# Optimization experiments

Measured on AMD Instinct MI355X. Metric: run time of the kernel, lower is better.

Reference implementation:

```python
import jax, jax.numpy as jnp
import numpy as np

N = 100000        # nodes
E = 1600000       # directed edges (avg degree 16)
F_IN, F_HID, F_OUT = 512, 32, 16


def setup_inputs() -> dict:
    key = jax.random.key(0)
    k0, k1, k2, k3 = jax.random.split(key, 4)
    x = jax.random.normal(k0, (N, F_IN), dtype=jnp.float32)
    edge_index = jax.random.randint(k1, (2, E), 0, N, dtype=jnp.int32)
    # Glorot-ish init for the two GCNConv linear weights
    W1 = jax.random.normal(k2, (F_IN, F_HID), dtype=jnp.float32) / np.float32(np.sqrt(F_IN))
    W2 = jax.random.normal(k3, (F_HID, F_OUT), dtype=jnp.float32) / np.float32(np.sqrt(F_HID))
    b1 = jnp.zeros((F_HID,), jnp.float32)
    b2 = jnp.zeros((F_OUT,), jnp.float32)
    return {"x": x, "W1": W1, "b1": b1, "W2": W2, "b2": b2, "edge_index": edge_index}


def gcn_conv(x, W, b, src, dst):
    """PyG GCNConv: h = x W; symmetric-normalized aggregation with self-loops; + bias."""
    h = x @ W                                   # [N, F_out] project first (PyG order)
    # degree including the implicit self-loop (start from ones)
    deg = jnp.ones((N,), h.dtype).at[dst].add(1.0)
    dinv = jax.lax.rsqrt(deg)                   # deg^{-1/2}
    coef = (dinv[src] * dinv[dst])[:, None]     # [E, 1] edge norm
    msg = h[src] * coef                         # gather + scale
    agg = jax.ops.segment_sum(msg, dst, num_segments=N)  # scatter-add to dst
    agg = agg + h * (dinv * dinv)[:, None]      # self-loop contribution
    return agg + b


def reference(x, W1, b1, W2, b2, edge_index):
    src, dst = edge_index[0], edge_index[1]
    h = jax.nn.relu(gcn_conv(x, W1, b1, src, dst))
    # F.dropout(training=self.training) is identity in eval mode
    h = gcn_conv(h, W2, b2, src, dst)
    return jax.nn.log_softmax(h, axis=1)
```

## Files before the change

### kernel.cpp

```cpp
#include <hip/hip_runtime.h>
#include <hip/hip_bf16.h>
#include <cstdint>

#define NN   100000
#define NE   1600000
#define FIN  512
#define FHID 32
#define FOUT 16

#define BSHIFT 8
#define BSIZE  256
#define NBUCK  391
#define EPB    2048
#define NCHUNK ((NE + EPB - 1) / EPB)

typedef float f32x4 __attribute__((ext_vector_type(4)));
typedef short s16x8 __attribute__((ext_vector_type(8)));
typedef short s16x4 __attribute__((ext_vector_type(4)));
typedef int   i32x4 __attribute__((ext_vector_type(4)));
typedef unsigned int u32;
typedef unsigned short u16;

__device__ __forceinline__ short f2bf(float f) {
  union { float f; uint32_t u; } v; v.f = f;
  uint32_t r = v.u + 0x7fffu + ((v.u >> 16) & 1u);
  return (short)(r >> 16);
}
__device__ __forceinline__ float bf2f(u16 u) {
  union { uint32_t u; float f; } v; v.u = (uint32_t)u << 16; return v.f;
}

__global__ __launch_bounds__(256) void k_hist(const int* __restrict__ dst,
                                              u32* __restrict__ bcount) {
  __shared__ u32 h[NBUCK];
  int tid = threadIdx.x;
  for (int i = tid; i < NBUCK; i += 256) h[i] = 0;
  __syncthreads();
  int base = blockIdx.x * EPB;
  #pragma unroll
  for (int i = 0; i < 2; ++i) {
    int e0 = base + (i * 256 + tid) * 4;
    if (e0 + 3 < NE) {
      i32x4 d4 = *(const i32x4*)(dst + e0);
      atomicAdd(&h[d4[0] >> BSHIFT], 1u);
      atomicAdd(&h[d4[1] >> BSHIFT], 1u);
      atomicAdd(&h[d4[2] >> BSHIFT], 1u);
      atomicAdd(&h[d4[3] >> BSHIFT], 1u);
    } else {
      for (int k = 0; k < 4; ++k)
        if (e0 + k < NE) atomicAdd(&h[dst[e0 + k] >> BSHIFT], 1u);
    }
  }
  __syncthreads();
  for (int i = tid; i < NBUCK; i += 256)
    if (h[i]) atomicAdd(&bcount[i], h[i]);
}

__global__ __launch_bounds__(512) void k_bscan(const u32* __restrict__ bc,
                                               u32* __restrict__ bstart,
                                               u32* __restrict__ bcur) {
  __shared__ u32 tmp[512];
  int tid = threadIdx.x;
  u32 v = (tid < NBUCK) ? bc[tid] : 0;
  tmp[tid] = v;
  __syncthreads();
  #pragma unroll
  for (int off = 1; off < 512; off <<= 1) {
    u32 t = (tid >= off) ? tmp[tid - off] : 0;
    __syncthreads();
    tmp[tid] += t;
    __syncthreads();
  }
  if (tid < NBUCK) { u32 e = tmp[tid] - v; bstart[tid] = e; bcur[tid] = e; }
  if (tid == 511) bstart[NBUCK] = tmp[511];
}

__global__ __launch_bounds__(512) void k_bin(const int* __restrict__ src,
                                             const int* __restrict__ dst,
                                             u32* __restrict__ bcur,
                                             u32* __restrict__ binned) {
  __shared__ u32 cnt[NBUCK];
  __shared__ u32 lofs[NBUCK];
  __shared__ u32 gbase[NBUCK];
  __shared__ u32 tmp[512];
  __shared__ u32 stage[EPB];
  __shared__ u16 sb[EPB];
  int tid = threadIdx.x;
  for (int i = tid; i < NBUCK; i += 512) cnt[i] = 0;
  __syncthreads();

  int base = blockIdx.x * EPB;
  int e0 = base + tid * 4;
  u32 vals[4];
  u32 ofs[4];
  int bks[4];
  if (e0 + 3 < NE) {
    i32x4 s4 = *(const i32x4*)(src + e0);
    i32x4 d4 = *(const i32x4*)(dst + e0);
    #pragma unroll
    for (int k = 0; k < 4; ++k) {
      int b = d4[k] >> BSHIFT;
      bks[k] = b;
      vals[k] = (u32)s4[k] | ((u32)(d4[k] & (BSIZE - 1)) << 17);
      ofs[k] = atomicAdd(&cnt[b], 1u);
    }
  } else {
    #pragma unroll
    for (int k = 0; k < 4; ++k) {
      int e = e0 + k;
      bool ok = e < NE;
      int s = 0, d = 0;
      if (ok) { s = src[e]; d = dst[e]; }
      int b = ok ? (d >> BSHIFT) : -1;
      bks[k] = b;
      vals[k] = (u32)s | ((u32)(d & (BSIZE - 1)) << 17);
      ofs[k] = ok ? atomicAdd(&cnt[b], 1u) : 0;
    }
  }
  __syncthreads();

  u32 cv = (tid < NBUCK) ? cnt[tid] : 0;
  tmp[tid] = cv;
  __syncthreads();
  #pragma unroll
  for (int off = 1; off < 512; off <<= 1) {
    u32 t = (tid >= off) ? tmp[tid - off] : 0;
    __syncthreads();
    tmp[tid] += t;
    __syncthreads();
  }
  if (tid < NBUCK) {
    lofs[tid] = tmp[tid] - cv;
    gbase[tid] = cv ? atomicAdd(&bcur[tid], cv) : 0;
  }
  __syncthreads();
  u32 total = tmp[511];
  __syncthreads();

  #pragma unroll
  for (int k = 0; k < 4; ++k) {
    if (bks[k] >= 0) {
      u32 sl = lofs[bks[k]] + ofs[k];
      stage[sl] = vals[k];
      sb[sl] = (u16)bks[k];
    }
  }
  __syncthreads();

  for (u32 s2 = tid; s2 < total; s2 += 512) {
    int b = sb[s2];
    binned[gbase[b] + (s2 - lofs[b])] = stage[s2];
  }
}

__global__ __launch_bounds__(256) void k_fin(const u32* __restrict__ binned,
                                             const u32* __restrict__ bstart,
                                             int* __restrict__ deg,
                                             int* __restrict__ rs,
                                             float* __restrict__ dinv,
                                             int* __restrict__ csr) {
  __shared__ u32 degl[BSIZE];
  __shared__ u32 rsl[BSIZE];
  int tid = threadIdx.x;
  int b = blockIdx.x;
  u32 start = bstart[b];
  u32 n = bstart[b + 1] - start;

  degl[tid] = 0;
  __syncthreads();
  for (u32 k = tid; k < n; k += 256)
    atomicAdd(&degl[binned[start + k] >> 17], 1u);
  __syncthreads();

  u32 v = degl[tid];
  rsl[tid] = v;
  __syncthreads();
  #pragma unroll
  for (int off = 1; off < 256; off <<= 1) {
    u32 t = (tid >= off) ? rsl[tid - off] : 0;
    __syncthreads();
    rsl[tid] += t;
    __syncthreads();
  }
  u32 e = rsl[tid] - v;
  __syncthreads();
  rsl[tid] = e;

  int g = b * BSIZE + tid;
  if (g < NN) {
    deg[g] = (int)v;
    rs[g] = (int)(start + e);
    dinv[g] = rsqrtf(1.0f + (float)v);
  }
  __syncthreads();

  for (u32 k = tid; k < n; k += 256) {
    u32 vv = binned[start + k];
    u32 pos = atomicAdd(&rsl[vv >> 17], 1u);
    csr[start + pos] = (int)(vv & 0x1FFFFu);
  }
}

__global__ __launch_bounds__(256) void k_gemm1(const float* __restrict__ x,
                                               const float* __restrict__ W1,
                                               const float* __restrict__ dinv,
                                               u16* __restrict__ Hs1) {
  __shared__ s16x8 Blds[16][2][64];
  const int tid = threadIdx.x;
  for (int it = 0; it < 64; ++it) {
    int flat = it * 256 + tid;
    int i  = flat & 7;
    int l  = (flat >> 3) & 63;
    int nt = (flat >> 9) & 1;
    int kt = flat >> 10;
    int k  = kt * 32 + ((l >> 4) << 3) + i;
    int n  = nt * 16 + (l & 15);
    ((short*)Blds)[flat] = f2bf(W1[k * 32 + n]);
  }
  __syncthreads();

  const int lane = tid & 63;
  const int wv   = tid >> 6;
  const int h    = lane >> 4;
  const int m    = lane & 15;
  const int wid  = blockIdx.x * 4 + wv;
  if (wid >= 3125) return;
  const int t0 = wid * 2;

  const float* xr0 = x + (size_t)(t0 * 16 + m) * FIN + h * 8;
  const float* xr1 = xr0 + (size_t)16 * FIN;

  f32x4 acc[2][2] = {};
  #pragma unroll
  for (int kt = 0; kt < 16; ++kt) {
    f32x4 a0 = *(const f32x4*)(xr0 + kt * 32);
    f32x4 a1 = *(const f32x4*)(xr0 + kt * 32 + 4);
    f32x4 c0 = *(const f32x4*)(xr1 + kt * 32);
    f32x4 c1 = *(const f32x4*)(xr1 + kt * 32 + 4);
    s16x8 b0 = Blds[kt][0][lane];
    s16x8 b1 = Blds[kt][1][lane];
    s16x8 af, cf;
    af[0]=f2bf(a0[0]); af[1]=f2bf(a0[1]); af[2]=f2bf(a0[2]); af[3]=f2bf(a0[3]);
    af[4]=f2bf(a1[0]); af[5]=f2bf(a1[1]); af[6]=f2bf(a1[2]); af[7]=f2bf(a1[3]);
    cf[0]=f2bf(c0[0]); cf[1]=f2bf(c0[1]); cf[2]=f2bf(c0[2]); cf[3]=f2bf(c0[3]);
    cf[4]=f2bf(c1[0]); cf[5]=f2bf(c1[1]); cf[6]=f2bf(c1[2]); cf[7]=f2bf(c1[3]);
    acc[0][0] = __builtin_amdgcn_mfma_f32_16x16x32_bf16(af, b0, acc[0][0], 0, 0, 0);
    acc[0][1] = __builtin_amdgcn_mfma_f32_16x16x32_bf16(af, b1, acc[0][1], 0, 0, 0);
    acc[1][0] = __builtin_amdgcn_mfma_f32_16x16x32_bf16(cf, b0, acc[1][0], 0, 0, 0);
    acc[1][1] = __builtin_amdgcn_mfma_f32_16x16x32_bf16(cf, b1, acc[1][1], 0, 0, 0);
  }
  #pragma unroll
  for (int rt = 0; rt < 2; ++rt) {
    #pragma unroll
    for (int r = 0; r < 4; ++r) {
      int row = (t0 + rt) * 16 + h * 4 + r;
      float di = dinv[row];
      u16* o = Hs1 + (size_t)row * FHID + m;
      o[0]  = (u16)f2bf(acc[rt][0][r] * di);
      o[16] = (u16)f2bf(acc[rt][1][r] * di);
    }
  }
}

__global__ __launch_bounds__(256) void k_gat1(const int* __restrict__ csr,
                                              const int* __restrict__ rs,
                                              const int* __restrict__ deg,
                                              const float* __restrict__ dinv,
                                              const float* __restrict__ b1,
                                              const float* __restrict__ W2,
                                              const u16* __restrict__ Hs1,
                                              u16* __restrict__ Hs2) {
  __shared__ float w[FHID * FOUT];
  for (int i = threadIdx.x; i < FHID * FOUT; i += 256) w[i] = W2[i];
  __syncthreads();

  int t = blockIdx.x * 256 + threadIdx.x;
  int d = t >> 2;
  if (d >= NN) return;
  int p = t & 3;
  int start = rs[d], n = deg[d];

  float a0[8], a1[8], a2[8], a3[8];
  {
    s16x8 v = *(const s16x8*)(Hs1 + (size_t)d * FHID + p * 8);
    #pragma unroll
    for (int k = 0; k < 8; ++k) {
      a0[k] = bf2f((u16)v[k]); a1[k] = 0.f; a2[k] = 0.f; a3[k] = 0.f;
    }
  }
  int j = 0;
  for (; j + 8 <= n; j += 8) {
    int s0 = csr[start + j];
    int s1 = csr[start + j + 1];
    int s2 = csr[start + j + 2];
    int s3 = csr[start + j + 3];
    int s4 = csr[start + j + 4];
    int s5 = csr[start + j + 5];
    int s6 = csr[start + j + 6];
    int s7 = csr[start + j + 7];
    s16x8 v0 = *(const s16x8*)(Hs1 + (size_t)s0 * FHID + p * 8);
    s16x8 v1 = *(const s16x8*)(Hs1 + (size_t)s1 * FHID + p * 8);
    s16x8 v2 = *(const s16x8*)(Hs1 + (size_t)s2 * FHID + p * 8);
    s16x8 v3 = *(const s16x8*)(Hs1 + (size_t)s3 * FHID + p * 8);
    s16x8 v4 = *(const s16x8*)(Hs1 + (size_t)s4 * FHID + p * 8);
    s16x8 v5 = *(const s16x8*)(Hs1 + (size_t)s5 * FHID + p * 8);
    s16x8 v6 = *(const s16x8*)(Hs1 + (size_t)s6 * FHID + p * 8);
    s16x8 v7 = *(const s16x8*)(Hs1 + (size_t)s7 * FHID + p * 8);
    #pragma unroll
    for (int k = 0; k < 8; ++k) {
      a0[k] += bf2f((u16)v0[k]);
      a1[k] += bf2f((u16)v1[k]);
      a2[k] += bf2f((u16)v2[k]);
      a3[k] += bf2f((u16)v3[k]);
      a0[k] += bf2f((u16)v4[k]);
      a1[k] += bf2f((u16)v5[k]);
      a2[k] += bf2f((u16)v6[k]);
      a3[k] += bf2f((u16)v7[k]);
    }
  }
  for (; j + 4 <= n; j += 4) {
    int s0 = csr[start + j];
    int s1 = csr[start + j + 1];
    int s2 = csr[start + j + 2];
    int s3 = csr[start + j + 3];
    s16x8 v0 = *(const s16x8*)(Hs1 + (size_t)s0 * FHID + p * 8);
    s16x8 v1 = *(const s16x8*)(Hs1 + (size_t)s1 * FHID + p * 8);
    s16x8 v2 = *(const s16x8*)(Hs1 + (size_t)s2 * FHID + p * 8);
    s16x8 v3 = *(const s16x8*)(Hs1 + (size_t)s3 * FHID + p * 8);
    #pragma unroll
    for (int k = 0; k < 8; ++k) {
      a0[k] += bf2f((u16)v0[k]);
      a1[k] += bf2f((u16)v1[k]);
      a2[k] += bf2f((u16)v2[k]);
      a3[k] += bf2f((u16)v3[k]);
    }
  }
  for (; j < n; ++j) {
    int s0 = csr[start + j];
    s16x8 v0 = *(const s16x8*)(Hs1 + (size_t)s0 * FHID + p * 8);
    #pragma unroll
    for (int k = 0; k < 8; ++k) a0[k] += bf2f((u16)v0[k]);
  }

  float dd = dinv[d];
  float h[8];
  #pragma unroll
  for (int k = 0; k < 8; ++k)
    h[k] = fmaxf(((a0[k] + a1[k]) + (a2[k] + a3[k])) * dd + b1[p * 8 + k], 0.0f);

  float pj[FOUT];
  #pragma unroll
  for (int jj = 0; jj < FOUT; ++jj) pj[jj] = 0.f;
  #pragma unroll
  for (int k = 0; k < 8; ++k)
    #pragma unroll
    for (int jj = 0; jj < FOUT; ++jj)
      pj[jj] = fmaf(h[k], w[(p * 8 + k) * FOUT + jj], pj[jj]);
  #pragma unroll
  for (int jj = 0; jj < FOUT; ++jj) {
    pj[jj] += __shfl_xor(pj[jj], 1);
    pj[jj] += __shfl_xor(pj[jj], 2);
  }
  s16x4 o;
  #pragma unroll
  for (int q = 0; q < 4; ++q) o[q] = f2bf(pj[p * 4 + q] * dd);
  *(s16x4*)(Hs2 + (size_t)d * FOUT + p * 4) = o;
}

__global__ __launch_bounds__(256) void k_gat2(const int* __restrict__ csr,
                                              const int* __restrict__ rs,
                                              const int* __restrict__ deg,
                                              const float* __restrict__ dinv,
                                              const float* __restrict__ b2,
                                              const u16* __restrict__ Hs2,
                                              float* __restrict__ out) {
  int t = blockIdx.x * 256 + threadIdx.x;
  int d = t >> 2;
  if (d >= NN) return;
  int p = t & 3;
  int start = rs[d], n = deg[d];

  float a0[4], a1[4], a2[4], a3[4];
  {
    s16x4 v = *(const s16x4*)(Hs2 + (size_t)d * FOUT + p * 4);
    #pragma unroll
    for (int k = 0; k < 4; ++k) {
      a0[k] = bf2f((u16)v[k]); a1[k] = 0.f; a2[k] = 0.f; a3[k] = 0.f;
    }
  }
  int j = 0;
  for (; j + 8 <= n; j += 8) {
    int s0 = csr[start + j];
    int s1 = csr[start + j + 1];
    int s2 = csr[start + j + 2];
    int s3 = csr[start + j + 3];
    int s4 = csr[start + j + 4];
    int s5 = csr[start + j + 5];
    int s6 = csr[start + j + 6];
    int s7 = csr[start + j + 7];
    s16x4 v0 = *(const s16x4*)(Hs2 + (size_t)s0 * FOUT + p * 4);
    s16x4 v1 = *(const s16x4*)(Hs2 + (size_t)s1 * FOUT + p * 4);
    s16x4 v2 = *(const s16x4*)(Hs2 + (size_t)s2 * FOUT + p * 4);
    s16x4 v3 = *(const s16x4*)(Hs2 + (size_t)s3 * FOUT + p * 4);
    s16x4 v4 = *(const s16x4*)(Hs2 + (size_t)s4 * FOUT + p * 4);
    s16x4 v5 = *(const s16x4*)(Hs2 + (size_t)s5 * FOUT + p * 4);
    s16x4 v6 = *(const s16x4*)(Hs2 + (size_t)s6 * FOUT + p * 4);
    s16x4 v7 = *(const s16x4*)(Hs2 + (size_t)s7 * FOUT + p * 4);
    #pragma unroll
    for (int k = 0; k < 4; ++k) {
      a0[k] += bf2f((u16)v0[k]);
      a1[k] += bf2f((u16)v1[k]);
      a2[k] += bf2f((u16)v2[k]);
      a3[k] += bf2f((u16)v3[k]);
      a0[k] += bf2f((u16)v4[k]);
      a1[k] += bf2f((u16)v5[k]);
      a2[k] += bf2f((u16)v6[k]);
      a3[k] += bf2f((u16)v7[k]);
    }
  }
  for (; j + 4 <= n; j += 4) {
    int s0 = csr[start + j];
    int s1 = csr[start + j + 1];
    int s2 = csr[start + j + 2];
    int s3 = csr[start + j + 3];
    s16x4 v0 = *(const s16x4*)(Hs2 + (size_t)s0 * FOUT + p * 4);
    s16x4 v1 = *(const s16x4*)(Hs2 + (size_t)s1 * FOUT + p * 4);
    s16x4 v2 = *(const s16x4*)(Hs2 + (size_t)s2 * FOUT + p * 4);
    s16x4 v3 = *(const s16x4*)(Hs2 + (size_t)s3 * FOUT + p * 4);
    #pragma unroll
    for (int k = 0; k < 4; ++k) {
      a0[k] += bf2f((u16)v0[k]);
      a1[k] += bf2f((u16)v1[k]);
      a2[k] += bf2f((u16)v2[k]);
      a3[k] += bf2f((u16)v3[k]);
    }
  }
  for (; j < n; ++j) {
    int s0 = csr[start + j];
    s16x4 v0 = *(const s16x4*)(Hs2 + (size_t)s0 * FOUT + p * 4);
    #pragma unroll
    for (int k = 0; k < 4; ++k) a0[k] += bf2f((u16)v0[k]);
  }

  float dd = dinv[d];
  float z[4];
  #pragma unroll
  for (int k = 0; k < 4; ++k)
    z[k] = ((a0[k] + a1[k]) + (a2[k] + a3[k])) * dd + b2[p * 4 + k];

  float m = fmaxf(fmaxf(z[0], z[1]), fmaxf(z[2], z[3]));
  m = fmaxf(m, __shfl_xor(m, 1));
  m = fmaxf(m, __shfl_xor(m, 2));
  float s = expf(z[0]-m) + expf(z[1]-m) + expf(z[2]-m) + expf(z[3]-m);
  s += __shfl_xor(s, 1);
  s += __shfl_xor(s, 2);
  float lse = m + logf(s);

  f32x4 o = { z[0]-lse, z[1]-lse, z[2]-lse, z[3]-lse };
  *(f32x4*)(out + (size_t)d * FOUT + p * 4) = o;
}

extern "C" void kernel_launch(void* const* d_in, const int* in_sizes, int n_in,
                              void* d_out, int out_size, void* d_ws, size_t ws_size,
                              hipStream_t stream) {
  const float* x  = (const float*)d_in[0];
  const float* W1 = (const float*)d_in[1];
  const float* b1 = (const float*)d_in[2];
  const float* W2 = (const float*)d_in[3];
  const float* b2 = (const float*)d_in[4];
  const int*   ei = (const int*)d_in[5];
  const int* srcv = ei;
  const int* dstv = ei + NE;

  char* ws = (char*)d_ws;
  const size_t KB = 1024, MB = 1048576;
  u32*   bcount = (u32*)(ws + 0);
  u32*   bstart = (u32*)(ws + 8 * KB);
  u32*   bcur   = (u32*)(ws + 16 * KB);
  int*   deg    = (int*)(ws + 512 * KB);
  int*   rs     = (int*)(ws + 1024 * KB);
  float* dinv   = (float*)(ws + 1536 * KB);
  u32*   binned = (u32*)(ws + 2 * MB);
  int*   csr    = (int*)(ws + 9 * MB);
  u16*   Hs1    = (u16*)(ws + 16 * MB);
  u16*   Hs2    = (u16*)(ws + 23 * MB);
  float* out    = (float*)d_out;

  hipMemsetAsync(bcount, 0, NBUCK * sizeof(u32), stream);

  k_hist <<<NCHUNK, 256, 0, stream>>>(dstv, bcount);
  k_bscan<<<1,      512, 0, stream>>>(bcount, bstart, bcur);
  k_bin  <<<NCHUNK, 512, 0, stream>>>(srcv, dstv, bcur, binned);
  k_fin  <<<NBUCK,  256, 0, stream>>>(binned, bstart, deg, rs, dinv, csr);
  k_gemm1<<<782, 256, 0, stream>>>(x, W1, dinv, Hs1);
  k_gat1 <<<(NN * 4 + 255) / 256, 256, 0, stream>>>(csr, rs, deg, dinv, b1, W2, Hs1, Hs2);
  k_gat2 <<<(NN * 4 + 255) / 256, 256, 0, stream>>>(csr, rs, deg, dinv, b2, Hs2, out);
}
```

Measured before the change: 164.3 us.

## Split layer-1 gather into two 16-wide halves, fuse bucket scan, enlarge buckets

Hidden features are written as two 16-column bf16 arrays, and the layer-1 gather runs as two passes that each gather one half. The first pass stores a partial fp32 projection, which the second pass adds to its own. The aim is to shrink the per-pass gather working set so it fits better in cache, at the cost of reading the CSR twice and an extra fp32 round trip. The bucket scan kernel is folded into the histogram kernel through a last-block ticket atomic, removing one launch. Buckets grow to 512 nodes, and the histogram blocks handle more edges each.

```diff
diff --git a/kernel.cpp b/kernel.cpp
--- a/kernel.cpp
+++ b/kernel.cpp
@@ -8,11 +8,13 @@
 #define FHID 32
 #define FOUT 16
 
-#define BSHIFT 8
-#define BSIZE  256
-#define NBUCK  391
-#define EPB    2048
-#define NCHUNK ((NE + EPB - 1) / EPB)
+#define BSHIFT 9
+#define BSIZE  512
+#define NBUCK  196
+#define HEPB   4096
+#define NHB    ((NE + HEPB - 1) / HEPB)
+#define BEPB   2048
+#define NBB    ((NE + BEPB - 1) / BEPB)
 
 typedef float f32x4 __attribute__((ext_vector_type(4)));
 typedef short s16x8 __attribute__((ext_vector_type(8)));
@@ -31,14 +33,18 @@
 }
 
 __global__ __launch_bounds__(256) void k_hist(const int* __restrict__ dst,
-                                              u32* __restrict__ bcount) {
-  __shared__ u32 h[NBUCK];
+                                              u32* __restrict__ bcount,
+                                              u32* __restrict__ ticket,
+                                              u32* __restrict__ bstart,
+                                              u32* __restrict__ bcur) {
+  __shared__ u32 h[256];
+  __shared__ bool amlast;
   int tid = threadIdx.x;
-  for (int i = tid; i < NBUCK; i += 256) h[i] = 0;
-  __syncthreads();
-  int base = blockIdx.x * EPB;
-  #pragma unroll
-  for (int i = 0; i < 2; ++i) {
+  h[tid] = 0;
+  __syncthreads();
+  int base = blockIdx.x * HEPB;
+  #pragma unroll
+  for (int i = 0; i < HEPB / 1024; ++i) {
     int e0 = base + (i * 256 + tid) * 4;
     if (e0 + 3 < NE) {
       i32x4 d4 = *(const i32x4*)(dst + e0);
@@ -52,27 +58,28 @@
     }
   }
   __syncthreads();
-  for (int i = tid; i < NBUCK; i += 256)
-    if (h[i]) atomicAdd(&bcount[i], h[i]);
-}
-
-__global__ __launch_bounds__(512) void k_bscan(const u32* __restrict__ bc,
-                                               u32* __restrict__ bstart,
-                                               u32* __restrict__ bcur) {
-  __shared__ u32 tmp[512];
-  int tid = threadIdx.x;
-  u32 v = (tid < NBUCK) ? bc[tid] : 0;
-  tmp[tid] = v;
-  __syncthreads();
-  #pragma unroll
-  for (int off = 1; off < 512; off <<= 1) {
-    u32 t = (tid >= off) ? tmp[tid - off] : 0;
+  if (tid < NBUCK && h[tid]) atomicAdd(&bcount[tid], h[tid]);
+  __syncthreads();
+  if (tid == 0) {
+    __threadfence();
+    u32 t = __hip_atomic_fetch_add(ticket, 1u, __ATOMIC_ACQ_REL, __HIP_MEMORY_SCOPE_AGENT);
+    amlast = (t == gridDim.x - 1);
+  }
+  __syncthreads();
+  if (!amlast) return;
+  u32 v = (tid < NBUCK)
+        ? __hip_atomic_load(&bcount[tid], __ATOMIC_RELAXED, __HIP_MEMORY_SCOPE_AGENT) : 0;
+  h[tid] = v;
+  __syncthreads();
+  #pragma unroll
+  for (int off = 1; off < 256; off <<= 1) {
+    u32 t = (tid >= off) ? h[tid - off] : 0;
     __syncthreads();
-    tmp[tid] += t;
+    h[tid] += t;
     __syncthreads();
   }
-  if (tid < NBUCK) { u32 e = tmp[tid] - v; bstart[tid] = e; bcur[tid] = e; }
-  if (tid == 511) bstart[NBUCK] = tmp[511];
+  if (tid < NBUCK) { u32 e = h[tid] - v; bstart[tid] = e; bcur[tid] = e; }
+  if (tid == 255) bstart[NBUCK] = h[255];
 }
 
 __global__ __launch_bounds__(512) void k_bin(const int* __restrict__ src,
@@ -83,17 +90,15 @@
   __shared__ u32 lofs[NBUCK];
   __shared__ u32 gbase[NBUCK];
   __shared__ u32 tmp[512];
-  __shared__ u32 stage[EPB];
-  __shared__ u16 sb[EPB];
+  __shared__ u32 stage[BEPB];
+  __shared__ u16 sb[BEPB];
   int tid = threadIdx.x;
   for (int i = tid; i < NBUCK; i += 512) cnt[i] = 0;
   __syncthreads();
 
-  int base = blockIdx.x * EPB;
+  int base = blockIdx.x * BEPB;
   int e0 = base + tid * 4;
-  u32 vals[4];
-  u32 ofs[4];
-  int bks[4];
+  u32 vals[4]; u32 ofs[4]; int bks[4];
   if (e0 + 3 < NE) {
     i32x4 s4 = *(const i32x4*)(src + e0);
     i32x4 d4 = *(const i32x4*)(dst + e0);
@@ -161,36 +166,44 @@
                                              int* __restrict__ csr) {
   __shared__ u32 degl[BSIZE];
   __shared__ u32 rsl[BSIZE];
+  __shared__ u32 tmp[256];
   int tid = threadIdx.x;
   int b = blockIdx.x;
   u32 start = bstart[b];
   u32 n = bstart[b + 1] - start;
 
-  degl[tid] = 0;
+  degl[tid] = 0; degl[tid + 256] = 0;
   __syncthreads();
   for (u32 k = tid; k < n; k += 256)
     atomicAdd(&degl[binned[start + k] >> 17], 1u);
   __syncthreads();
 
-  u32 v = degl[tid];
-  rsl[tid] = v;
+  u32 a0 = degl[2 * tid], a1 = degl[2 * tid + 1];
+  u32 s = a0 + a1;
+  tmp[tid] = s;
   __syncthreads();
   #pragma unroll
   for (int off = 1; off < 256; off <<= 1) {
-    u32 t = (tid >= off) ? rsl[tid - off] : 0;
+    u32 t = (tid >= off) ? tmp[tid - off] : 0;
     __syncthreads();
-    rsl[tid] += t;
+    tmp[tid] += t;
     __syncthreads();
   }
-  u32 e = rsl[tid] - v;
-  __syncthreads();
-  rsl[tid] = e;
-
-  int g = b * BSIZE + tid;
-  if (g < NN) {
-    deg[g] = (int)v;
-    rs[g] = (int)(start + e);
-    dinv[g] = rsqrtf(1.0f + (float)v);
+  u32 e = tmp[tid] - s;
+  rsl[2 * tid] = e;
+  rsl[2 * tid + 1] = e + a0;
+  __syncthreads();
+
+  #pragma unroll
+  for (int q = 0; q < 2; ++q) {
+    int t = tid + q * 256;
+    int g = b * BSIZE + t;
+    if (g < NN) {
+      u32 dg = degl[t];
+      deg[g] = (int)dg;
+      rs[g] = (int)(start + rsl[t]);
+      dinv[g] = rsqrtf(1.0f + (float)dg);
+    }
   }
   __syncthreads();
 
@@ -204,7 +217,8 @@
 __global__ __launch_bounds__(256) void k_gemm1(const float* __restrict__ x,
                                                const float* __restrict__ W1,
                                                const float* __restrict__ dinv,
-                                               u16* __restrict__ Hs1) {
+                                               u16* __restrict__ Hs1a,
+                                               u16* __restrict__ Hs1b) {
   __shared__ s16x8 Blds[16][2][64];
   const int tid = threadIdx.x;
   for (int it = 0; it < 64; ++it) {
@@ -255,115 +269,159 @@
     for (int r = 0; r < 4; ++r) {
       int row = (t0 + rt) * 16 + h * 4 + r;
       float di = dinv[row];
-      u16* o = Hs1 + (size_t)row * FHID + m;
-      o[0]  = (u16)f2bf(acc[rt][0][r] * di);
-      o[16] = (u16)f2bf(acc[rt][1][r] * di);
-    }
-  }
-}
-
-__global__ __launch_bounds__(256) void k_gat1(const int* __restrict__ csr,
-                                              const int* __restrict__ rs,
-                                              const int* __restrict__ deg,
-                                              const float* __restrict__ dinv,
-                                              const float* __restrict__ b1,
-                                              const float* __restrict__ W2,
-                                              const u16* __restrict__ Hs1,
-                                              u16* __restrict__ Hs2) {
-  __shared__ float w[FHID * FOUT];
-  for (int i = threadIdx.x; i < FHID * FOUT; i += 256) w[i] = W2[i];
-  __syncthreads();
-
+      Hs1a[(size_t)row * 16 + m] = (u16)f2bf(acc[rt][0][r] * di);
+      Hs1b[(size_t)row * 16 + m] = (u16)f2bf(acc[rt][1][r] * di);
+    }
+  }
+}
+
+__global__ __launch_bounds__(256) void k_gat1a(const int* __restrict__ csr,
+                                               const int* __restrict__ rs,
+                                               const int* __restrict__ deg,
+                                               const float* __restrict__ dinv,
+                                               const float* __restrict__ b1,
+                                               const float* __restrict__ W2,
+                                               const u16* __restrict__ Hs1a,
+                                               float* __restrict__ P2) {
+  __shared__ float w[256];
+  w[threadIdx.x] = W2[threadIdx.x];
+  __syncthreads();
   int t = blockIdx.x * 256 + threadIdx.x;
   int d = t >> 2;
   if (d >= NN) return;
   int p = t & 3;
   int start = rs[d], n = deg[d];
 
-  float a0[8], a1[8], a2[8], a3[8];
+  float a0[4], a1[4], a2[4], a3[4];
   {
-    s16x8 v = *(const s16x8*)(Hs1 + (size_t)d * FHID + p * 8);
-    #pragma unroll
-    for (int k = 0; k < 8; ++k) {
-      a0[k] = bf2f((u16)v[k]); a1[k] = 0.f; a2[k] = 0.f; a3[k] = 0.f;
-    }
+    s16x4 v = *(const s16x4*)(Hs1a + (size_t)d * 16 + p * 4);
+    #pragma unroll
+    for (int k = 0; k < 4; ++k) { a0[k] = bf2f((u16)v[k]); a1[k]=0.f; a2[k]=0.f; a3[k]=0.f; }
   }
   int j = 0;
   for (; j + 8 <= n; j += 8) {
-    int s0 = csr[start + j];
-    int s1 = csr[start + j + 1];
-    int s2 = csr[start + j + 2];
-    int s3 = csr[start + j + 3];
-    int s4 = csr[start + j + 4];
-    int s5 = csr[start + j + 5];
-    int s6 = csr[start + j + 6];
-    int s7 = csr[start + j + 7];
-    s16x8 v0 = *(const s16x8*)(Hs1 + (size_t)s0 * FHID + p * 8);
-    s16x8 v1 = *(const s16x8*)(Hs1 + (size_t)s1 * FHID + p * 8);
-    s16x8 v2 = *(const s16x8*)(Hs1 + (size_t)s2 * FHID + p * 8);
-    s16x8 v3 = *(const s16x8*)(Hs1 + (size_t)s3 * FHID + p * 8);
-    s16x8 v4 = *(const s16x8*)(Hs1 + (size_t)s4 * FHID + p * 8);
-    s16x8 v5 = *(const s16x8*)(Hs1 + (size_t)s5 * FHID + p * 8);
-    s16x8 v6 = *(const s16x8*)(Hs1 + (size_t)s6 * FHID + p * 8);
-    s16x8 v7 = *(const s16x8*)(Hs1 + (size_t)s7 * FHID + p * 8);
-    #pragma unroll
-    for (int k = 0; k < 8; ++k) {
-      a0[k] += bf2f((u16)v0[k]);
-      a1[k] += bf2f((u16)v1[k]);
-      a2[k] += bf2f((u16)v2[k]);
-      a3[k] += bf2f((u16)v3[k]);
-      a0[k] += bf2f((u16)v4[k]);
-      a1[k] += bf2f((u16)v5[k]);
-      a2[k] += bf2f((u16)v6[k]);
-      a3[k] += bf2f((u16)v7[k]);
-    }
-  }
-  for (; j + 4 <= n; j += 4) {
-    int s0 = csr[start + j];
-    int s1 = csr[start + j + 1];
-    int s2 = csr[start + j + 2];
-    int s3 = csr[start + j + 3];
-    s16x8 v0 = *(const s16x8*)(Hs1 + (size_t)s0 * FHID + p * 8);
-    s16x8 v1 = *(const s16x8*)(Hs1 + (size_t)s1 * FHID + p * 8);
-    s16x8 v2 = *(const s16x8*)(Hs1 + (size_t)s2 * FHID + p * 8);
-    s16x8 v3 = *(const s16x8*)(Hs1 + (size_t)s3 * FHID + p * 8);
-    #pragma unroll
-    for (int k = 0; k < 8; ++k) {
-      a0[k] += bf2f((u16)v0[k]);
-      a1[k] += bf2f((u16)v1[k]);
-      a2[k] += bf2f((u16)v2[k]);
-      a3[k] += bf2f((u16)v3[k]);
+    int s0=csr[start+j],   s1=csr[start+j+1], s2=csr[start+j+2], s3=csr[start+j+3];
+    int s4=csr[start+j+4], s5=csr[start+j+5], s6=csr[start+j+6], s7=csr[start+j+7];
+    s16x4 v0 = *(const s16x4*)(Hs1a + (size_t)s0 * 16 + p * 4);
+    s16x4 v1 = *(const s16x4*)(Hs1a + (size_t)s1 * 16 + p * 4);
+    s16x4 v2 = *(const s16x4*)(Hs1a + (size_t)s2 * 16 + p * 4);
+    s16x4 v3 = *(const s16x4*)(Hs1a + (size_t)s3 * 16 + p * 4);
+    s16x4 v4 = *(const s16x4*)(Hs1a + (size_t)s4 * 16 + p * 4);
+    s16x4 v5 = *(const s16x4*)(Hs1a + (size_t)s5 * 16 + p * 4);
+    s16x4 v6 = *(const s16x4*)(Hs1a + (size_t)s6 * 16 + p * 4);
+    s16x4 v7 = *(const s16x4*)(Hs1a + (size_t)s7 * 16 + p * 4);
+    #pragma unroll
+    for (int k = 0; k < 4; ++k) {
+      a0[k] += bf2f((u16)v0[k]); a1[k] += bf2f((u16)v1[k]);
+      a2[k] += bf2f((u16)v2[k]); a3[k] += bf2f((u16)v3[k]);
+      a0[k] += bf2f((u16)v4[k]); a1[k] += bf2f((u16)v5[k]);
+      a2[k] += bf2f((u16)v6[k]); a3[k] += bf2f((u16)v7[k]);
     }
   }
   for (; j < n; ++j) {
     int s0 = csr[start + j];
-    s16x8 v0 = *(const s16x8*)(Hs1 + (size_t)s0 * FHID + p * 8);
-    #pragma unroll
-    for (int k = 0; k < 8; ++k) a0[k] += bf2f((u16)v0[k]);
+    s16x4 v0 = *(const s16x4*)(Hs1a + (size_t)s0 * 16 + p * 4);
+    #pragma unroll
+    for (int k = 0; k < 4; ++k) a0[k] += bf2f((u16)v0[k]);
   }
 
   float dd = dinv[d];
-  float h[8];
-  #pragma unroll
-  for (int k = 0; k < 8; ++k)
-    h[k] = fmaxf(((a0[k] + a1[k]) + (a2[k] + a3[k])) * dd + b1[p * 8 + k], 0.0f);
+  float h[4];
+  #pragma unroll
+  for (int k = 0; k < 4; ++k)
+    h[k] = fmaxf(((a0[k]+a1[k]) + (a2[k]+a3[k])) * dd + b1[p * 4 + k], 0.0f);
 
   float pj[FOUT];
   #pragma unroll
   for (int jj = 0; jj < FOUT; ++jj) pj[jj] = 0.f;
   #pragma unroll
-  for (int k = 0; k < 8; ++k)
+  for (int k = 0; k < 4; ++k)
     #pragma unroll
     for (int jj = 0; jj < FOUT; ++jj)
-      pj[jj] = fmaf(h[k], w[(p * 8 + k) * FOUT + jj], pj[jj]);
+      pj[jj] = fmaf(h[k], w[(p * 4 + k) * FOUT + jj], pj[jj]);
   #pragma unroll
   for (int jj = 0; jj < FOUT; ++jj) {
     pj[jj] += __shfl_xor(pj[jj], 1);
     pj[jj] += __shfl_xor(pj[jj], 2);
   }
+  f32x4 o = { pj[p*4+0], pj[p*4+1], pj[p*4+2], pj[p*4+3] };
+  *(f32x4*)(P2 + (size_t)d * FOUT + p * 4) = o;
+}
+
+__global__ __launch_bounds__(256) void k_gat1b(const int* __restrict__ csr,
+                                               const int* __restrict__ rs,
+                                               const int* __restrict__ deg,
+                                               const float* __restrict__ dinv,
+                                               const float* __restrict__ b1,
+                                               const float* __restrict__ W2,
+                                               const u16* __restrict__ Hs1b,
+                                               const float* __restrict__ P2,
+                                               u16* __restrict__ Hs2) {
+  __shared__ float w[256];
+  w[threadIdx.x] = W2[256 + threadIdx.x];
+  __syncthreads();
+  int t = blockIdx.x * 256 + threadIdx.x;
+  int d = t >> 2;
+  if (d >= NN) return;
+  int p = t & 3;
+  int start = rs[d], n = deg[d];
+
+  float a0[4], a1[4], a2[4], a3[4];
+  {
+    s16x4 v = *(const s16x4*)(Hs1b + (size_t)d * 16 + p * 4);
+    #pragma unroll
+    for (int k = 0; k < 4; ++k) { a0[k] = bf2f((u16)v[k]); a1[k]=0.f; a2[k]=0.f; a3[k]=0.f; }
+  }
+  int j = 0;
+  for (; j + 8 <= n; j += 8) {
+    int s0=csr[start+j],   s1=csr[start+j+1], s2=csr[start+j+2], s3=csr[start+j+3];
+    int s4=csr[start+j+4], s5=csr[start+j+5], s6=csr[start+j+6], s7=csr[start+j+7];
+    s16x4 v0 = *(const s16x4*)(Hs1b + (size_t)s0 * 16 + p * 4);
+    s16x4 v1 = *(const s16x4*)(Hs1b + (size_t)s1 * 16 + p * 4);
+    s16x4 v2 = *(const s16x4*)(Hs1b + (size_t)s2 * 16 + p * 4);
+    s16x4 v3 = *(const s16x4*)(Hs1b + (size_t)s3 * 16 + p * 4);
+    s16x4 v4 = *(const s16x4*)(Hs1b + (size_t)s4 * 16 + p * 4);
+    s16x4 v5 = *(const s16x4*)(Hs1b + (size_t)s5 * 16 + p * 4);
+    s16x4 v6 = *(const s16x4*)(Hs1b + (size_t)s6 * 16 + p * 4);
+    s16x4 v7 = *(const s16x4*)(Hs1b + (size_t)s7 * 16 + p * 4);
+    #pragma unroll
+    for (int k = 0; k < 4; ++k) {
+      a0[k] += bf2f((u16)v0[k]); a1[k] += bf2f((u16)v1[k]);
+      a2[k] += bf2f((u16)v2[k]); a3[k] += bf2f((u16)v3[k]);
+      a0[k] += bf2f((u16)v4[k]); a1[k] += bf2f((u16)v5[k]);
+      a2[k] += bf2f((u16)v6[k]); a3[k] += bf2f((u16)v7[k]);
+    }
+  }
+  for (; j < n; ++j) {
+    int s0 = csr[start + j];
+    s16x4 v0 = *(const s16x4*)(Hs1b + (size_t)s0 * 16 + p * 4);
+    #pragma unroll
+    for (int k = 0; k < 4; ++k) a0[k] += bf2f((u16)v0[k]);
+  }
+
+  float dd = dinv[d];
+  float h[4];
+  #pragma unroll
+  for (int k = 0; k < 4; ++k)
+    h[k] = fmaxf(((a0[k]+a1[k]) + (a2[k]+a3[k])) * dd + b1[16 + p * 4 + k], 0.0f);
+
+  float pj[FOUT];
+  #pragma unroll
+  for (int jj = 0; jj < FOUT; ++jj) pj[jj] = 0.f;
+  #pragma unroll
+  for (int k = 0; k < 4; ++k)
+    #pragma unroll
+    for (int jj = 0; jj < FOUT; ++jj)
+      pj[jj] = fmaf(h[k], w[(p * 4 + k) * FOUT + jj], pj[jj]);
+  #pragma unroll
+  for (int jj = 0; jj < FOUT; ++jj) {
+    pj[jj] += __shfl_xor(pj[jj], 1);
+    pj[jj] += __shfl_xor(pj[jj], 2);
+  }
+  f32x4 prev = *(const f32x4*)(P2 + (size_t)d * FOUT + p * 4);
   s16x4 o;
   #pragma unroll
-  for (int q = 0; q < 4; ++q) o[q] = f2bf(pj[p * 4 + q] * dd);
+  for (int q = 0; q < 4; ++q) o[q] = f2bf((pj[p*4+q] + prev[q]) * dd);
   *(s16x4*)(Hs2 + (size_t)d * FOUT + p * 4) = o;
 }
 
@@ -384,20 +442,12 @@
   {
     s16x4 v = *(const s16x4*)(Hs2 + (size_t)d * FOUT + p * 4);
     #pragma unroll
-    for (int k = 0; k < 4; ++k) {
-      a0[k] = bf2f((u16)v[k]); a1[k] = 0.f; a2[k] = 0.f; a3[k] = 0.f;
-    }
+    for (int k = 0; k < 4; ++k) { a0[k] = bf2f((u16)v[k]); a1[k]=0.f; a2[k]=0.f; a3[k]=0.f; }
   }
   int j = 0;
   for (; j + 8 <= n; j += 8) {
-    int s0 = csr[start + j];
-    int s1 = csr[start + j + 1];
-    int s2 = csr[start + j + 2];
-    int s3 = csr[start + j + 3];
-    int s4 = csr[start + j + 4];
-    int s5 = csr[start + j + 5];
-    int s6 = csr[start + j + 6];
-    int s7 = csr[start + j + 7];
+    int s0=csr[start+j],   s1=csr[start+j+1], s2=csr[start+j+2], s3=csr[start+j+3];
+    int s4=csr[start+j+4], s5=csr[start+j+5], s6=csr[start+j+6], s7=csr[start+j+7];
     s16x4 v0 = *(const s16x4*)(Hs2 + (size_t)s0 * FOUT + p * 4);
     s16x4 v1 = *(const s16x4*)(Hs2 + (size_t)s1 * FOUT + p * 4);
     s16x4 v2 = *(const s16x4*)(Hs2 + (size_t)s2 * FOUT + p * 4);
@@ -408,31 +458,10 @@
     s16x4 v7 = *(const s16x4*)(Hs2 + (size_t)s7 * FOUT + p * 4);
     #pragma unroll
     for (int k = 0; k < 4; ++k) {
-      a0[k] += bf2f((u16)v0[k]);
-      a1[k] += bf2f((u16)v1[k]);
-      a2[k] += bf2f((u16)v2[k]);
-      a3[k] += bf2f((u16)v3[k]);
-      a0[k] += bf2f((u16)v4[k]);
-      a1[k] += bf2f((u16)v5[k]);
-      a2[k] += bf2f((u16)v6[k]);
-      a3[k] += bf2f((u16)v7[k]);
-    }
-  }
-  for (; j + 4 <= n; j += 4) {
-    int s0 = csr[start + j];
-    int s1 = csr[start + j + 1];
-    int s2 = csr[start + j + 2];
-    int s3 = csr[start + j + 3];
-    s16x4 v0 = *(const s16x4*)(Hs2 + (size_t)s0 * FOUT + p * 4);
-    s16x4 v1 = *(const s16x4*)(Hs2 + (size_t)s1 * FOUT + p * 4);
-    s16x4 v2 = *(const s16x4*)(Hs2 + (size_t)s2 * FOUT + p * 4);
-    s16x4 v3 = *(const s16x4*)(Hs2 + (size_t)s3 * FOUT + p * 4);
-    #pragma unroll
-    for (int k = 0; k < 4; ++k) {
-      a0[k] += bf2f((u16)v0[k]);
-      a1[k] += bf2f((u16)v1[k]);
-      a2[k] += bf2f((u16)v2[k]);
-      a3[k] += bf2f((u16)v3[k]);
+      a0[k] += bf2f((u16)v0[k]); a1[k] += bf2f((u16)v1[k]);
+      a2[k] += bf2f((u16)v2[k]); a3[k] += bf2f((u16)v3[k]);
+      a0[k] += bf2f((u16)v4[k]); a1[k] += bf2f((u16)v5[k]);
+      a2[k] += bf2f((u16)v6[k]); a3[k] += bf2f((u16)v7[k]);
     }
   }
   for (; j < n; ++j) {
@@ -446,7 +475,7 @@
   float z[4];
   #pragma unroll
   for (int k = 0; k < 4; ++k)
-    z[k] = ((a0[k] + a1[k]) + (a2[k] + a3[k])) * dd + b2[p * 4 + k];
+    z[k] = ((a0[k]+a1[k]) + (a2[k]+a3[k])) * dd + b2[p * 4 + k];
 
   float m = fmaxf(fmaxf(z[0], z[1]), fmaxf(z[2], z[3]));
   m = fmaxf(m, __shfl_xor(m, 1));
@@ -475,6 +504,7 @@
   char* ws = (char*)d_ws;
   const size_t KB = 1024, MB = 1048576;
   u32*   bcount = (u32*)(ws + 0);
+  u32*   ticket = (u32*)(ws + 1 * KB);
   u32*   bstart = (u32*)(ws + 8 * KB);
   u32*   bcur   = (u32*)(ws + 16 * KB);
   int*   deg    = (int*)(ws + 512 * KB);
@@ -482,17 +512,19 @@
   float* dinv   = (float*)(ws + 1536 * KB);
   u32*   binned = (u32*)(ws + 2 * MB);
   int*   csr    = (int*)(ws + 9 * MB);
-  u16*   Hs1    = (u16*)(ws + 16 * MB);
-  u16*   Hs2    = (u16*)(ws + 23 * MB);
+  u16*   Hs1a   = (u16*)(ws + 16 * MB);
+  u16*   Hs1b   = (u16*)(ws + 20 * MB);
+  u16*   Hs2    = (u16*)(ws + 24 * MB);
+  float* P2     = (float*)(ws + 28 * MB);
   float* out    = (float*)d_out;
 
-  hipMemsetAsync(bcount, 0, NBUCK * sizeof(u32), stream);
-
-  k_hist <<<NCHUNK, 256, 0, stream>>>(dstv, bcount);
-  k_bscan<<<1,      512, 0, stream>>>(bcount, bstart, bcur);
-  k_bin  <<<NCHUNK, 512, 0, stream>>>(srcv, dstv, bcur, binned);
-  k_fin  <<<NBUCK,  256, 0, stream>>>(binned, bstart, deg, rs, dinv, csr);
-  k_gemm1<<<782, 256, 0, stream>>>(x, W1, dinv, Hs1);
-  k_gat1 <<<(NN * 4 + 255) / 256, 256, 0, stream>>>(csr, rs, deg, dinv, b1, W2, Hs1, Hs2);
+  hipMemsetAsync(ws, 0, 2 * KB, stream);
+
+  k_hist <<<NHB, 256, 0, stream>>>(dstv, bcount, ticket, bstart, bcur);
+  k_bin  <<<NBB, 512, 0, stream>>>(srcv, dstv, bcur, binned);
+  k_fin  <<<NBUCK, 256, 0, stream>>>(binned, bstart, deg, rs, dinv, csr);
+  k_gemm1<<<782, 256, 0, stream>>>(x, W1, dinv, Hs1a, Hs1b);
+  k_gat1a<<<(NN * 4 + 255) / 256, 256, 0, stream>>>(csr, rs, deg, dinv, b1, W2, Hs1a, P2);
+  k_gat1b<<<(NN * 4 + 255) / 256, 256, 0, stream>>>(csr, rs, deg, dinv, b1, W2, Hs1b, P2, Hs2);
   k_gat2 <<<(NN * 4 + 255) / 256, 256, 0, stream>>>(csr, rs, deg, dinv, b2, Hs2, out);
 }
```

Result: slower. 177.4 us (+8.0%).
